# Optimization experiments

Hardware: AMD Instinct MI355X
Metric: run time of the kernel (lower is better)

## Reference

```python
import jax, jax.numpy as jnp
import numpy as np

N, CIN, COUT, E, NDIR = 65536, 128, 128, 589824, 9


def sel_conv(x, src, dst, sel, W, b):
    # x: [N, Cin]; W: [D, Cin, Cout]; edges j->i: out[i] += x[j] @ W[sel]
    n = x.shape[0]
    xs = x[src]  # [E, Cin] gather
    out = jnp.zeros((n, W.shape[2]), x.dtype)
    for d in range(W.shape[0]):  # fixed small direction count (9 or 1)
        m = (sel == d).astype(x.dtype)[:, None]
        agg = jax.ops.segment_sum(xs * m, dst, num_segments=n)  # [N, Cin]
        out = out + agg @ W[d]
    return out + b


def bn_eval(x, g, be, rm, rv, eps=1e-5):
    return (x - rm) * (g * jax.lax.rsqrt(rv + eps)) + be


def setup_inputs() -> dict:
    key = jax.random.key(0)
    ks = jax.random.split(key, 24)
    s = 0.05
    inp = {
        "x": jax.random.normal(ks[0], (N, CIN), jnp.float32),
        "edge_index": jax.random.randint(ks[1], (2, E), 0, N),
        "selections": jax.random.randint(ks[2], (E,), 0, NDIR),
        "W1": jax.random.normal(ks[3], (NDIR, CIN, COUT), jnp.float32) * s,
        "b1": jax.random.normal(ks[4], (COUT,), jnp.float32) * s,
        "g1": 1.0 + jax.random.normal(ks[5], (COUT,), jnp.float32) * s,
        "be1": jax.random.normal(ks[6], (COUT,), jnp.float32) * s,
        "rm1": jax.random.normal(ks[7], (COUT,), jnp.float32) * s,
        "rv1": 0.5 + jax.random.uniform(ks[8], (COUT,), jnp.float32),
        "W2": jax.random.normal(ks[9], (NDIR, COUT, COUT), jnp.float32) * s,
        "b2": jax.random.normal(ks[10], (COUT,), jnp.float32) * s,
        "g2": 1.0 + jax.random.normal(ks[11], (COUT,), jnp.float32) * s,
        "be2": jax.random.normal(ks[12], (COUT,), jnp.float32) * s,
        "rm2": jax.random.normal(ks[13], (COUT,), jnp.float32) * s,
        "rv2": 0.5 + jax.random.uniform(ks[14], (COUT,), jnp.float32),
        "W3": jax.random.normal(ks[15], (1, CIN, COUT), jnp.float32) * s,
        "b3": jax.random.normal(ks[16], (COUT,), jnp.float32) * s,
        "g3": 1.0 + jax.random.normal(ks[17], (COUT,), jnp.float32) * s,
        "be3": jax.random.normal(ks[18], (COUT,), jnp.float32) * s,
        "rm3": jax.random.normal(ks[19], (COUT,), jnp.float32) * s,
        "rv3": 0.5 + jax.random.uniform(ks[20], (COUT,), jnp.float32),
    }
    return inp


def reference(x, edge_index, selections, W1, b1, g1, be1, rm1, rv1,
              W2, b2, g2, be2, rm2, rv2, W3, b3, g3, be3, rm3, rv3):
    src, dst = edge_index[0], edge_index[1]
    # conv1: SelectionConv(3x3) + BN + ELU
    h = jax.nn.elu(bn_eval(sel_conv(x, src, dst, selections, W1, b1), g1, be1, rm1, rv1))
    # conv2: SelectionConv(3x3) + BN + ELU
    h = jax.nn.elu(bn_eval(sel_conv(h, src, dst, selections, W2, b2), g2, be2, rm2, rv2))
    # conv3: SelectionConv(1x1) shortcut (only selection-0 edges)
    sc = sel_conv(x, src, dst, selections, W3, b3)
    return jax.nn.elu(bn_eval(h + sc, g3, be3, rm3, rv3))
```

## Files before the change

### kernel.cpp

```cpp
#include <hip/hip_runtime.h>
#include <hip/hip_bf16.h>
#include <math.h>

#define N_NODES 65536
#define NDIR 9
#define NEDGE 589824
#define NBINS (N_NODES*NDIR)
#define TILE_M 32
#define SKEY_CAP 1024

typedef __attribute__((ext_vector_type(8))) short short8;
typedef __attribute__((ext_vector_type(4))) float f32x4;

__device__ inline float bf2f(unsigned short u){ return __uint_as_float(((unsigned int)u)<<16); }
__device__ inline unsigned short f2bf(float f){
  unsigned int x = __float_as_uint(f);
  x += 0x7fff + ((x>>16)&1);
  return (unsigned short)(x>>16);
}
__device__ inline float elu1(float x){ return x>0.f ? x : expm1f(x); }

__global__ void prep_w(const float* __restrict__ W1, const float* __restrict__ W2,
                       const float* __restrict__ W3,
                       const float* __restrict__ g1, const float* __restrict__ rv1,
                       const float* __restrict__ g2, const float* __restrict__ rv2,
                       const float* __restrict__ g3, const float* __restrict__ rv3,
                       unsigned short* __restrict__ Wt1, unsigned short* __restrict__ Wt2){
  int idx = blockIdx.x*256 + threadIdx.x;
  const float eps = 1e-5f;
  if (idx < 1280*128) {
    int n = idx >> 7, k = idx & 127;
    float v;
    if (n < 1152) { int d = n >> 7, c = n & 127;
      float s = g1[c]*rsqrtf(rv1[c]+eps); v = W1[(d*128 + k)*128 + c] * s; }
    else { int c = n - 1152;
      float s = g3[c]*rsqrtf(rv3[c]+eps); v = W3[k*128 + c] * s; }
    Wt1[idx] = f2bf(v);
  } else {
    int j = idx - 1280*128;
    int n = j >> 7, k = j & 127;
    int d = n >> 7, c = n & 127;
    float s = g2[c]*rsqrtf(rv2[c]+eps);
    Wt2[j] = f2bf(W2[(d*128 + k)*128 + c] * s);
  }
}

__global__ void prep_bias(const float* b1,const float* g1,const float* be1,const float* rm1,const float* rv1,
                          const float* b2,const float* g2,const float* be2,const float* rm2,const float* rv2,
                          const float* b3,const float* g3,const float* be3,const float* rm3,const float* rv3,
                          float* bias1, float* bias2, float* bias3, float* s3v){
  int c = threadIdx.x;
  const float eps = 1e-5f;
  float s1 = g1[c]*rsqrtf(rv1[c]+eps);
  bias1[c] = (b1[c]-rm1[c])*s1 + be1[c];
  float s2 = g2[c]*rsqrtf(rv2[c]+eps);
  bias2[c] = (b2[c]-rm2[c])*s2 + be2[c];
  float s3 = g3[c]*rsqrtf(rv3[c]+eps);
  bias3[c] = (b3[c]-rm3[c])*s3 + be3[c];
  s3v[c] = s3;
}

__global__ void xcast_k(const float* __restrict__ x, unsigned short* __restrict__ xb){
  int i = (blockIdx.x*256 + threadIdx.x)*8;
  f32x4 f0 = *(const f32x4*)(x + i);
  f32x4 f1 = *(const f32x4*)(x + i + 4);
  short8 t;
  #pragma unroll
  for (int j = 0; j < 4; j++){ t[j] = (short)f2bf(f0[j]); t[4+j] = (short)f2bf(f1[j]); }
  *(short8*)(xb + i) = t;
}

__global__ void hist_k(const int* __restrict__ dst, const int* __restrict__ sel,
                       int* __restrict__ hist){
  int e = blockIdx.x*256 + threadIdx.x;
  atomicAdd(&hist[dst[e]*9 + sel[e]], 1);
}

__global__ void scan1_k(const int* __restrict__ in, int* __restrict__ out, int* __restrict__ bsum){
  __shared__ int wsum[4];
  int t = threadIdx.x;
  int base = blockIdx.x*1024 + t*4;
  int4 v = *(const int4*)(in + base);
  int s = v.x + v.y + v.z + v.w;
  int lane = t & 63, w = t >> 6;
  int inc = s;
  #pragma unroll
  for (int o = 1; o < 64; o <<= 1){ int n = __shfl_up(inc, o); if (lane >= o) inc += n; }
  if (lane == 63) wsum[w] = inc;
  __syncthreads();
  int acc = 0;
  for (int i = 0; i < w; i++) acc += wsum[i];
  int ex = acc + inc - s;
  out[base] = ex; out[base+1] = ex + v.x; out[base+2] = ex + v.x + v.y; out[base+3] = ex + v.x + v.y + v.z;
  if (t == 255) bsum[blockIdx.x] = acc + inc;
}

__global__ void scan3_k(int* __restrict__ rs, const int* __restrict__ bsumx, int* __restrict__ cursor){
  int i = blockIdx.x*256 + threadIdx.x;
  int v = rs[i] + bsumx[i >> 10];
  rs[i] = v; cursor[i] = v;
  if (i == 0) rs[NBINS] = NEDGE;
}

__global__ void scatter_k(const int* __restrict__ src, const int* __restrict__ dst,
                          const int* __restrict__ sel,
                          int* __restrict__ cursor, int* __restrict__ sorted){
  int e = blockIdx.x*256 + threadIdx.x;
  int bin = dst[e]*9 + sel[e];
  int pos = atomicAdd(&cursor[bin], 1);
  sorted[pos] = src[e];
}

__device__ __forceinline__ void mfma_tile(f32x4 acc[2][2],
                                          const unsigned short* agg,
                                          const unsigned short* __restrict__ Wd,
                                          int w, int q, int r){
  #pragma unroll
  for (int kk = 0; kk < 4; kk++){
    const unsigned short* wp = Wd + (size_t)(w*32 + r)*128 + kk*32 + q*8;
    short8 b0 = *(const short8*)wp;
    short8 b1 = *(const short8*)(wp + 16*128);
    #pragma unroll
    for (int mt = 0; mt < 2; mt++){
      short8 av = *(const short8*)&agg[(mt*16 + r)*136 + kk*32 + q*8];
      acc[mt][0] = __builtin_amdgcn_mfma_f32_16x16x32_bf16(av, b0, acc[mt][0], 0, 0, 0);
      acc[mt][1] = __builtin_amdgcn_mfma_f32_16x16x32_bf16(av, b1, acc[mt][1], 0, 0, 0);
    }
  }
}

template<int IS_L2>
__global__ __launch_bounds__(256, 8) void layer_k(
    const unsigned short* __restrict__ H,
    const unsigned short* __restrict__ X,
    const unsigned short* __restrict__ Wf,
    const unsigned short* __restrict__ W3f,
    const int* __restrict__ rs, const int* __restrict__ sorted,
    const float* __restrict__ biasA, const float* __restrict__ bias3,
    const float* __restrict__ s3v,
    unsigned short* __restrict__ outB, float* __restrict__ outF){
  __shared__ __align__(16) unsigned short agg[TILE_M*136];
  __shared__ int skey[SKEY_CAP];
  __shared__ int rsl[TILE_M*9 + 1];
  const int tid = threadIdx.x;
  const int w = tid >> 6, lane = tid & 63;
  const int q = lane >> 4, r = lane & 15;
  const int rid = tid >> 4, c = tid & 15;
  const int m0 = blockIdx.x * TILE_M;

  for (int i = tid; i <= TILE_M*9; i += 256) rsl[i] = rs[m0*9 + i];
  __syncthreads();
  const int lo = rsl[0];
  const int cnt = rsl[TILE_M*9] - lo;
  for (int i = tid; i < cnt && i < SKEY_CAP; i += 256) skey[i] = sorted[lo + i];

  f32x4 acc[2][2];
  #pragma unroll
  for (int mt = 0; mt < 2; mt++){ acc[mt][0] = (f32x4){0,0,0,0}; acc[mt][1] = (f32x4){0,0,0,0}; }

  #pragma unroll 1
  for (int d = 0; d < 9; d++){
    __syncthreads();
    #pragma unroll
    for (int t = 0; t < 2; t++){
      int nl = t*16 + rid;
      int b = nl*9 + d;
      int s = rsl[b] - lo, e = rsl[b+1] - lo;
      f32x4 a0 = {0,0,0,0}, a1 = {0,0,0,0};
      for (int i = s; i < e; i++){
        int key = (i < SKEY_CAP) ? skey[i] : sorted[lo + i];
        short8 v = *(const short8*)(H + (size_t)key*128 + c*8);
        a0[0] += bf2f((unsigned short)v[0]); a0[1] += bf2f((unsigned short)v[1]);
        a0[2] += bf2f((unsigned short)v[2]); a0[3] += bf2f((unsigned short)v[3]);
        a1[0] += bf2f((unsigned short)v[4]); a1[1] += bf2f((unsigned short)v[5]);
        a1[2] += bf2f((unsigned short)v[6]); a1[3] += bf2f((unsigned short)v[7]);
      }
      short8 o;
      o[0]=(short)f2bf(a0[0]); o[1]=(short)f2bf(a0[1]); o[2]=(short)f2bf(a0[2]); o[3]=(short)f2bf(a0[3]);
      o[4]=(short)f2bf(a1[0]); o[5]=(short)f2bf(a1[1]); o[6]=(short)f2bf(a1[2]); o[7]=(short)f2bf(a1[3]);
      *(short8*)&agg[nl*136 + c*8] = o;
    }
    __syncthreads();
    mfma_tile(acc, agg, Wf + (size_t)d*128*128, w, q, r);
  }

  if constexpr (!IS_L2){
    #pragma unroll
    for (int mt = 0; mt < 2; mt++)
      #pragma unroll
      for (int n2 = 0; n2 < 2; n2++){
        int col = w*32 + n2*16 + r;
        float bA = biasA[col];
        #pragma unroll
        for (int rr = 0; rr < 4; rr++){
          int row = m0 + mt*16 + q*4 + rr;
          outB[(size_t)row*128 + col] = f2bf(elu1(acc[mt][n2][rr] + bA));
        }
      }
  } else {
    f32x4 sca[2][2];
    #pragma unroll
    for (int mt = 0; mt < 2; mt++){ sca[mt][0] = (f32x4){0,0,0,0}; sca[mt][1] = (f32x4){0,0,0,0}; }
    __syncthreads();
    #pragma unroll
    for (int t = 0; t < 2; t++){
      int nl = t*16 + rid;
      int b = nl*9;
      int s = rsl[b] - lo, e = rsl[b+1] - lo;
      f32x4 a0 = {0,0,0,0}, a1 = {0,0,0,0};
      for (int i = s; i < e; i++){
        int key = (i < SKEY_CAP) ? skey[i] : sorted[lo + i];
        short8 v = *(const short8*)(X + (size_t)key*128 + c*8);
        a0[0] += bf2f((unsigned short)v[0]); a0[1] += bf2f((unsigned short)v[1]);
        a0[2] += bf2f((unsigned short)v[2]); a0[3] += bf2f((unsigned short)v[3]);
        a1[0] += bf2f((unsigned short)v[4]); a1[1] += bf2f((unsigned short)v[5]);
        a1[2] += bf2f((unsigned short)v[6]); a1[3] += bf2f((unsigned short)v[7]);
      }
      short8 o;
      o[0]=(short)f2bf(a0[0]); o[1]=(short)f2bf(a0[1]); o[2]=(short)f2bf(a0[2]); o[3]=(short)f2bf(a0[3]);
      o[4]=(short)f2bf(a1[0]); o[5]=(short)f2bf(a1[1]); o[6]=(short)f2bf(a1[2]); o[7]=(short)f2bf(a1[3]);
      *(short8*)&agg[nl*136 + c*8] = o;
    }
    __syncthreads();
    mfma_tile(sca, agg, W3f, w, q, r);
    #pragma unroll
    for (int mt = 0; mt < 2; mt++)
      #pragma unroll
      for (int n2 = 0; n2 < 2; n2++){
        int col = w*32 + n2*16 + r;
        float bA = biasA[col], b3 = bias3[col], s3 = s3v[col];
        #pragma unroll
        for (int rr = 0; rr < 4; rr++){
          int row = m0 + mt*16 + q*4 + rr;
          float h = elu1(acc[mt][n2][rr] + bA);
          outF[(size_t)row*128 + col] = elu1(h*s3 + sca[mt][n2][rr] + b3);
        }
      }
  }
}

extern "C" void kernel_launch(void* const* d_in, const int* in_sizes, int n_in,
                              void* d_out, int out_size, void* d_ws, size_t ws_size,
                              hipStream_t stream){
  const float* x   = (const float*)d_in[0];
  const int*   ei  = (const int*)d_in[1];
  const int*   sel = (const int*)d_in[2];
  const float* W1  = (const float*)d_in[3];
  const float* b1  = (const float*)d_in[4];
  const float* g1  = (const float*)d_in[5];
  const float* be1 = (const float*)d_in[6];
  const float* rm1 = (const float*)d_in[7];
  const float* rv1 = (const float*)d_in[8];
  const float* W2  = (const float*)d_in[9];
  const float* b2  = (const float*)d_in[10];
  const float* g2  = (const float*)d_in[11];
  const float* be2 = (const float*)d_in[12];
  const float* rm2 = (const float*)d_in[13];
  const float* rv2 = (const float*)d_in[14];
  const float* W3  = (const float*)d_in[15];
  const float* b3  = (const float*)d_in[16];
  const float* g3  = (const float*)d_in[17];
  const float* be3 = (const float*)d_in[18];
  const float* rm3 = (const float*)d_in[19];
  const float* rv3 = (const float*)d_in[20];

  char* ws = (char*)d_ws;
  unsigned short* xb   = (unsigned short*)(ws);
  unsigned short* h1   = (unsigned short*)(ws + 16777216);
  unsigned short* Wt1  = (unsigned short*)(ws + 33554432);
  unsigned short* Wt2  = (unsigned short*)(ws + 33882112);
  float* bias1  = (float*)(ws + 34177024);
  float* bias2  = bias1 + 128;
  float* bias3  = bias1 + 256;
  float* s3v    = bias1 + 384;
  int* hist     = (int*)(ws + 34179072);
  int* rs       = (int*)(ws + 36538368);
  int* cursor   = (int*)(ws + 38897920);
  int* bsum     = (int*)(ws + 41257216);
  int* bsumx    = (int*)(ws + 41261312);
  int* bsumT    = (int*)(ws + 41265408);
  int* sorted   = (int*)(ws + 41265664);

  const int* srcp = ei;
  const int* dstp = ei + NEDGE;

  hipMemsetAsync(hist, 0, NBINS*sizeof(int), stream);
  prep_w<<<1216, 256, 0, stream>>>(W1, W2, W3, g1, rv1, g2, rv2, g3, rv3, Wt1, Wt2);
  prep_bias<<<1, 128, 0, stream>>>(b1,g1,be1,rm1,rv1, b2,g2,be2,rm2,rv2, b3,g3,be3,rm3,rv3,
                                   bias1, bias2, bias3, s3v);
  xcast_k<<<4096, 256, 0, stream>>>(x, xb);
  hist_k<<<NEDGE/256, 256, 0, stream>>>(dstp, sel, hist);
  scan1_k<<<NBINS/1024, 256, 0, stream>>>(hist, rs, bsum);
  scan1_k<<<1, 256, 0, stream>>>(bsum, bsumx, bsumT);
  scan3_k<<<NBINS/256, 256, 0, stream>>>(rs, bsumx, cursor);
  scatter_k<<<NEDGE/256, 256, 0, stream>>>(srcp, dstp, sel, cursor, sorted);

  layer_k<0><<<2048, 256, 0, stream>>>(xb, nullptr, Wt1, nullptr, rs, sorted,
                                       bias1, nullptr, nullptr, h1, nullptr);
  layer_k<1><<<2048, 256, 0, stream>>>(h1, xb, Wt2, Wt1 + 1152*128, rs, sorted,
                                       bias2, bias3, s3v, nullptr, (float*)d_out);
}
```

Baseline: 369.9 us.

## Gather all nine directions in one pass with unrolled loads and 512-thread blocks

The layer kernel now gathers all nine direction aggregates for a 32-node tile in a single sweep over each node's sorted edge list. Each thread issues four independent row loads per iteration and writes a per-direction result into a larger shared buffer, so the nine gather/sync/MFMA rounds become one gather phase followed by nine MFMA steps. Blocks grow to 512 threads with one node row per 16-lane group, and each wave computes a 16x32 output tile. The aim is more memory-level parallelism and fewer barriers, at the cost of a much larger LDS footprint (about 78 KB per block), lower occupancy, and a smaller shared key cache.

New measurement: 506.4 us. 1.37x slower.

```diff
diff --git a/kernel.cpp b/kernel.cpp
--- a/kernel.cpp
+++ b/kernel.cpp
@@ -7,7 +7,8 @@
 #define NEDGE 589824
 #define NBINS (N_NODES*NDIR)
 #define TILE_M 32
-#define SKEY_CAP 1024
+#define SKEY_CAP 448
+#define APITCH 136
 
 typedef __attribute__((ext_vector_type(8))) short short8;
 typedef __attribute__((ext_vector_type(4))) float f32x4;
@@ -111,26 +112,8 @@
   sorted[pos] = src[e];
 }
 
-__device__ __forceinline__ void mfma_tile(f32x4 acc[2][2],
-                                          const unsigned short* agg,
-                                          const unsigned short* __restrict__ Wd,
-                                          int w, int q, int r){
-  #pragma unroll
-  for (int kk = 0; kk < 4; kk++){
-    const unsigned short* wp = Wd + (size_t)(w*32 + r)*128 + kk*32 + q*8;
-    short8 b0 = *(const short8*)wp;
-    short8 b1 = *(const short8*)(wp + 16*128);
-    #pragma unroll
-    for (int mt = 0; mt < 2; mt++){
-      short8 av = *(const short8*)&agg[(mt*16 + r)*136 + kk*32 + q*8];
-      acc[mt][0] = __builtin_amdgcn_mfma_f32_16x16x32_bf16(av, b0, acc[mt][0], 0, 0, 0);
-      acc[mt][1] = __builtin_amdgcn_mfma_f32_16x16x32_bf16(av, b1, acc[mt][1], 0, 0, 0);
-    }
-  }
-}
-
 template<int IS_L2>
-__global__ __launch_bounds__(256, 8) void layer_k(
+__global__ __launch_bounds__(512, 4) void layer_k(
     const unsigned short* __restrict__ H,
     const unsigned short* __restrict__ X,
     const unsigned short* __restrict__ Wf,
@@ -139,103 +122,147 @@
     const float* __restrict__ biasA, const float* __restrict__ bias3,
     const float* __restrict__ s3v,
     unsigned short* __restrict__ outB, float* __restrict__ outF){
-  __shared__ __align__(16) unsigned short agg[TILE_M*136];
+  __shared__ __align__(16) unsigned short agg[NDIR*TILE_M*APITCH];
   __shared__ int skey[SKEY_CAP];
   __shared__ int rsl[TILE_M*9 + 1];
   const int tid = threadIdx.x;
   const int w = tid >> 6, lane = tid & 63;
   const int q = lane >> 4, r = lane & 15;
-  const int rid = tid >> 4, c = tid & 15;
+  const int nl = tid >> 4, c = tid & 15;
   const int m0 = blockIdx.x * TILE_M;
 
-  for (int i = tid; i <= TILE_M*9; i += 256) rsl[i] = rs[m0*9 + i];
+  for (int i = tid; i <= TILE_M*9; i += 512) rsl[i] = rs[m0*9 + i];
   __syncthreads();
   const int lo = rsl[0];
   const int cnt = rsl[TILE_M*9] - lo;
-  for (int i = tid; i < cnt && i < SKEY_CAP; i += 256) skey[i] = sorted[lo + i];
-
-  f32x4 acc[2][2];
-  #pragma unroll
-  for (int mt = 0; mt < 2; mt++){ acc[mt][0] = (f32x4){0,0,0,0}; acc[mt][1] = (f32x4){0,0,0,0}; }
-
-  #pragma unroll 1
-  for (int d = 0; d < 9; d++){
-    __syncthreads();
-    #pragma unroll
-    for (int t = 0; t < 2; t++){
-      int nl = t*16 + rid;
-      int b = nl*9 + d;
-      int s = rsl[b] - lo, e = rsl[b+1] - lo;
-      f32x4 a0 = {0,0,0,0}, a1 = {0,0,0,0};
-      for (int i = s; i < e; i++){
-        int key = (i < SKEY_CAP) ? skey[i] : sorted[lo + i];
-        short8 v = *(const short8*)(H + (size_t)key*128 + c*8);
+  for (int i = tid; i < cnt && i < SKEY_CAP; i += 512) skey[i] = sorted[lo + i];
+  __syncthreads();
+
+  {
+    const int b0 = nl*9;
+    const int s  = rsl[b0] - lo;
+    const int e9 = rsl[b0+9] - lo;
+    f32x4 a0 = (f32x4){0,0,0,0}, a1 = (f32x4){0,0,0,0};
+    int d = 0;
+    int nb = rsl[b0+1] - lo;
+
+    auto flushdir = [&](int dd){
+      short8 o;
+      o[0]=(short)f2bf(a0[0]); o[1]=(short)f2bf(a0[1]); o[2]=(short)f2bf(a0[2]); o[3]=(short)f2bf(a0[3]);
+      o[4]=(short)f2bf(a1[0]); o[5]=(short)f2bf(a1[1]); o[6]=(short)f2bf(a1[2]); o[7]=(short)f2bf(a1[3]);
+      *(short8*)&agg[((dd<<5) + nl)*APITCH + c*8] = o;
+      a0 = (f32x4){0,0,0,0}; a1 = (f32x4){0,0,0,0};
+    };
+    auto consume = [&](short8 v, int idx){
+      if (idx < e9) {
+        while (idx >= nb) { flushdir(d); d++; nb = rsl[b0 + d + 1] - lo; }
         a0[0] += bf2f((unsigned short)v[0]); a0[1] += bf2f((unsigned short)v[1]);
         a0[2] += bf2f((unsigned short)v[2]); a0[3] += bf2f((unsigned short)v[3]);
         a1[0] += bf2f((unsigned short)v[4]); a1[1] += bf2f((unsigned short)v[5]);
         a1[2] += bf2f((unsigned short)v[6]); a1[3] += bf2f((unsigned short)v[7]);
       }
+    };
+
+    for (int i = s; i < e9; i += 4) {
+      int j1 = (i+1 < e9) ? i+1 : i;
+      int j2 = (i+2 < e9) ? i+2 : i;
+      int j3 = (i+3 < e9) ? i+3 : i;
+      int k0 = (i  < SKEY_CAP) ? skey[i]  : sorted[lo + i];
+      int k1 = (j1 < SKEY_CAP) ? skey[j1] : sorted[lo + j1];
+      int k2 = (j2 < SKEY_CAP) ? skey[j2] : sorted[lo + j2];
+      int k3 = (j3 < SKEY_CAP) ? skey[j3] : sorted[lo + j3];
+      short8 v0 = *(const short8*)(H + (size_t)k0*128 + c*8);
+      short8 v1 = *(const short8*)(H + (size_t)k1*128 + c*8);
+      short8 v2 = *(const short8*)(H + (size_t)k2*128 + c*8);
+      short8 v3 = *(const short8*)(H + (size_t)k3*128 + c*8);
+      consume(v0, i); consume(v1, i+1); consume(v2, i+2); consume(v3, i+3);
+    }
+    for (; d < 9; d++) flushdir(d);
+  }
+  __syncthreads();
+
+  const int wr = (w & 1) * 16;
+  const int wc = (w >> 1) * 32;
+  f32x4 acc[2];
+  acc[0] = (f32x4){0,0,0,0}; acc[1] = (f32x4){0,0,0,0};
+  for (int d = 0; d < 9; d++){
+    const unsigned short* ag = agg + ((d<<5) + wr + r)*APITCH;
+    const unsigned short* Wd = Wf + (size_t)d*128*128 + (size_t)(wc + r)*128;
+    #pragma unroll
+    for (int kk = 0; kk < 4; kk++){
+      short8 av = *(const short8*)(ag + kk*32 + q*8);
+      short8 b0 = *(const short8*)(Wd + kk*32 + q*8);
+      short8 b1 = *(const short8*)(Wd + 16*128 + kk*32 + q*8);
+      acc[0] = __builtin_amdgcn_mfma_f32_16x16x32_bf16(av, b0, acc[0], 0, 0, 0);
+      acc[1] = __builtin_amdgcn_mfma_f32_16x16x32_bf16(av, b1, acc[1], 0, 0, 0);
+    }
+  }
+
+  if constexpr (!IS_L2){
+    #pragma unroll
+    for (int n2 = 0; n2 < 2; n2++){
+      int col = wc + n2*16 + r;
+      float bA = biasA[col];
+      #pragma unroll
+      for (int rr = 0; rr < 4; rr++){
+        int row = m0 + wr + q*4 + rr;
+        outB[(size_t)row*128 + col] = f2bf(elu1(acc[n2][rr] + bA));
+      }
+    }
+  } else {
+    __syncthreads();
+    {
+      const int b0 = nl*9;
+      const int s = rsl[b0] - lo, e = rsl[b0+1] - lo;
+      f32x4 a0 = (f32x4){0,0,0,0}, a1 = (f32x4){0,0,0,0};
+      for (int i = s; i < e; i += 2) {
+        int j1 = (i+1 < e) ? i+1 : i;
+        int k0 = (i  < SKEY_CAP) ? skey[i]  : sorted[lo + i];
+        int k1 = (j1 < SKEY_CAP) ? skey[j1] : sorted[lo + j1];
+        short8 v0 = *(const short8*)(X + (size_t)k0*128 + c*8);
+        short8 v1 = *(const short8*)(X + (size_t)k1*128 + c*8);
+        a0[0] += bf2f((unsigned short)v0[0]); a0[1] += bf2f((unsigned short)v0[1]);
+        a0[2] += bf2f((unsigned short)v0[2]); a0[3] += bf2f((unsigned short)v0[3]);
+        a1[0] += bf2f((unsigned short)v0[4]); a1[1] += bf2f((unsigned short)v0[5]);
+        a1[2] += bf2f((unsigned short)v0[6]); a1[3] += bf2f((unsigned short)v0[7]);
+        if (i+1 < e) {
+          a0[0] += bf2f((unsigned short)v1[0]); a0[1] += bf2f((unsigned short)v1[1]);
+          a0[2] += bf2f((unsigned short)v1[2]); a0[3] += bf2f((unsigned short)v1[3]);
+          a1[0] += bf2f((unsigned short)v1[4]); a1[1] += bf2f((unsigned short)v1[5]);
+          a1[2] += bf2f((unsigned short)v1[6]); a1[3] += bf2f((unsigned short)v1[7]);
+        }
+      }
       short8 o;
       o[0]=(short)f2bf(a0[0]); o[1]=(short)f2bf(a0[1]); o[2]=(short)f2bf(a0[2]); o[3]=(short)f2bf(a0[3]);
       o[4]=(short)f2bf(a1[0]); o[5]=(short)f2bf(a1[1]); o[6]=(short)f2bf(a1[2]); o[7]=(short)f2bf(a1[3]);
-      *(short8*)&agg[nl*136 + c*8] = o;
+      *(short8*)&agg[nl*APITCH + c*8] = o;
     }
     __syncthreads();
-    mfma_tile(acc, agg, Wf + (size_t)d*128*128, w, q, r);
-  }
-
-  if constexpr (!IS_L2){
+    f32x4 sca[2];
+    sca[0] = (f32x4){0,0,0,0}; sca[1] = (f32x4){0,0,0,0};
+    {
+      const unsigned short* ag = agg + (wr + r)*APITCH;
+      const unsigned short* Wd = W3f + (size_t)(wc + r)*128;
+      #pragma unroll
+      for (int kk = 0; kk < 4; kk++){
+        short8 av = *(const short8*)(ag + kk*32 + q*8);
+        short8 b0 = *(const short8*)(Wd + kk*32 + q*8);
+        short8 b1 = *(const short8*)(Wd + 16*128 + kk*32 + q*8);
+        sca[0] = __builtin_amdgcn_mfma_f32_16x16x32_bf16(av, b0, sca[0], 0, 0, 0);
+        sca[1] = __builtin_amdgcn_mfma_f32_16x16x32_bf16(av, b1, sca[1], 0, 0, 0);
+      }
+    }
     #pragma unroll
-    for (int mt = 0; mt < 2; mt++)
+    for (int n2 = 0; n2 < 2; n2++){
+      int col = wc + n2*16 + r;
+      float bA = biasA[col], b3 = bias3[col], s3 = s3v[col];
       #pragma unroll
-      for (int n2 = 0; n2 < 2; n2++){
-        int col = w*32 + n2*16 + r;
-        float bA = biasA[col];
-        #pragma unroll
-        for (int rr = 0; rr < 4; rr++){
-          int row = m0 + mt*16 + q*4 + rr;
-          outB[(size_t)row*128 + col] = f2bf(elu1(acc[mt][n2][rr] + bA));
-        }
-      }
-  } else {
-    f32x4 sca[2][2];
-    #pragma unroll
-    for (int mt = 0; mt < 2; mt++){ sca[mt][0] = (f32x4){0,0,0,0}; sca[mt][1] = (f32x4){0,0,0,0}; }
-    __syncthreads();
-    #pragma unroll
-    for (int t = 0; t < 2; t++){
-      int nl = t*16 + rid;
-      int b = nl*9;
-      int s = rsl[b] - lo, e = rsl[b+1] - lo;
-      f32x4 a0 = {0,0,0,0}, a1 = {0,0,0,0};
-      for (int i = s; i < e; i++){
-        int key = (i < SKEY_CAP) ? skey[i] : sorted[lo + i];
-        short8 v = *(const short8*)(X + (size_t)key*128 + c*8);
-        a0[0] += bf2f((unsigned short)v[0]); a0[1] += bf2f((unsigned short)v[1]);
-        a0[2] += bf2f((unsigned short)v[2]); a0[3] += bf2f((unsigned short)v[3]);
-        a1[0] += bf2f((unsigned short)v[4]); a1[1] += bf2f((unsigned short)v[5]);
-        a1[2] += bf2f((unsigned short)v[6]); a1[3] += bf2f((unsigned short)v[7]);
-      }
-      short8 o;
-      o[0]=(short)f2bf(a0[0]); o[1]=(short)f2bf(a0[1]); o[2]=(short)f2bf(a0[2]); o[3]=(short)f2bf(a0[3]);
-      o[4]=(short)f2bf(a1[0]); o[5]=(short)f2bf(a1[1]); o[6]=(short)f2bf(a1[2]); o[7]=(short)f2bf(a1[3]);
-      *(short8*)&agg[nl*136 + c*8] = o;
-    }
-    __syncthreads();
-    mfma_tile(sca, agg, W3f, w, q, r);
-    #pragma unroll
-    for (int mt = 0; mt < 2; mt++)
-      #pragma unroll
-      for (int n2 = 0; n2 < 2; n2++){
-        int col = w*32 + n2*16 + r;
-        float bA = biasA[col], b3 = bias3[col], s3 = s3v[col];
-        #pragma unroll
-        for (int rr = 0; rr < 4; rr++){
-          int row = m0 + mt*16 + q*4 + rr;
-          float h = elu1(acc[mt][n2][rr] + bA);
-          outF[(size_t)row*128 + col] = elu1(h*s3 + sca[mt][n2][rr] + b3);
-        }
-      }
+      for (int rr = 0; rr < 4; rr++){
+        int row = m0 + wr + q*4 + rr;
+        float h = elu1(acc[n2][rr] + bA);
+        outF[(size_t)row*128 + col] = elu1(h*s3 + sca[n2][rr] + b3);
+      }
+    }
   }
 }
 
@@ -295,8 +322,8 @@
   scan3_k<<<NBINS/256, 256, 0, stream>>>(rs, bsumx, cursor);
   scatter_k<<<NEDGE/256, 256, 0, stream>>>(srcp, dstp, sel, cursor, sorted);
 
-  layer_k<0><<<2048, 256, 0, stream>>>(xb, nullptr, Wt1, nullptr, rs, sorted,
+  layer_k<0><<<2048, 512, 0, stream>>>(xb, nullptr, Wt1, nullptr, rs, sorted,
                                        bias1, nullptr, nullptr, h1, nullptr);
-  layer_k<1><<<2048, 256, 0, stream>>>(h1, xb, Wt2, Wt1 + 1152*128, rs, sorted,
+  layer_k<1><<<2048, 512, 0, stream>>>(h1, xb, Wt2, Wt1 + 1152*128, rs, sorted,
                                        bias2, bias3, s3v, nullptr, (float*)d_out);
 }
```

## Double-buffer aggregation tile and interleave two row gathers per thread

Applied to the files above, without the earlier changes.

Adds a second LDS aggregation buffer, alternated by direction parity, so one barrier per direction suffices instead of two. The two rows handled by each thread are now gathered in a single interleaved loop, putting two independent global loads in flight per iteration. The shortcut gather writes to the other buffer. Launch bounds drop from 8 to 7 waves to allow the extra LDS and registers. The interleaved loop runs to the longer of the two segments and masks the shorter one, which can waste a load.

Measured after the change: 417.1 us. 1.13x slower.

```diff
diff --git a/kernel.cpp b/kernel.cpp
--- a/kernel.cpp
+++ b/kernel.cpp
@@ -8,6 +8,7 @@
 #define NBINS (N_NODES*NDIR)
 #define TILE_M 32
 #define SKEY_CAP 1024
+#define APITCH 136
 
 typedef __attribute__((ext_vector_type(8))) short short8;
 typedef __attribute__((ext_vector_type(4))) float f32x4;
@@ -122,7 +123,7 @@
     short8 b1 = *(const short8*)(wp + 16*128);
     #pragma unroll
     for (int mt = 0; mt < 2; mt++){
-      short8 av = *(const short8*)&agg[(mt*16 + r)*136 + kk*32 + q*8];
+      short8 av = *(const short8*)&agg[(mt*16 + r)*APITCH + kk*32 + q*8];
       acc[mt][0] = __builtin_amdgcn_mfma_f32_16x16x32_bf16(av, b0, acc[mt][0], 0, 0, 0);
       acc[mt][1] = __builtin_amdgcn_mfma_f32_16x16x32_bf16(av, b1, acc[mt][1], 0, 0, 0);
     }
@@ -130,7 +131,7 @@
 }
 
 template<int IS_L2>
-__global__ __launch_bounds__(256, 8) void layer_k(
+__global__ __launch_bounds__(256, 7) void layer_k(
     const unsigned short* __restrict__ H,
     const unsigned short* __restrict__ X,
     const unsigned short* __restrict__ Wf,
@@ -139,7 +140,7 @@
     const float* __restrict__ biasA, const float* __restrict__ bias3,
     const float* __restrict__ s3v,
     unsigned short* __restrict__ outB, float* __restrict__ outF){
-  __shared__ __align__(16) unsigned short agg[TILE_M*136];
+  __shared__ __align__(16) unsigned short agg[2*TILE_M*APITCH];
   __shared__ int skey[SKEY_CAP];
   __shared__ int rsl[TILE_M*9 + 1];
   const int tid = threadIdx.x;
@@ -153,6 +154,7 @@
   const int lo = rsl[0];
   const int cnt = rsl[TILE_M*9] - lo;
   for (int i = tid; i < cnt && i < SKEY_CAP; i += 256) skey[i] = sorted[lo + i];
+  __syncthreads();
 
   f32x4 acc[2][2];
   #pragma unroll
@@ -160,28 +162,46 @@
 
   #pragma unroll 1
   for (int d = 0; d < 9; d++){
-    __syncthreads();
-    #pragma unroll
-    for (int t = 0; t < 2; t++){
-      int nl = t*16 + rid;
-      int b = nl*9 + d;
-      int s = rsl[b] - lo, e = rsl[b+1] - lo;
-      f32x4 a0 = {0,0,0,0}, a1 = {0,0,0,0};
-      for (int i = s; i < e; i++){
-        int key = (i < SKEY_CAP) ? skey[i] : sorted[lo + i];
-        short8 v = *(const short8*)(H + (size_t)key*128 + c*8);
-        a0[0] += bf2f((unsigned short)v[0]); a0[1] += bf2f((unsigned short)v[1]);
-        a0[2] += bf2f((unsigned short)v[2]); a0[3] += bf2f((unsigned short)v[3]);
-        a1[0] += bf2f((unsigned short)v[4]); a1[1] += bf2f((unsigned short)v[5]);
-        a1[2] += bf2f((unsigned short)v[6]); a1[3] += bf2f((unsigned short)v[7]);
+    unsigned short* buf = agg + (d & 1)*(TILE_M*APITCH);
+    {
+      int bA = rid*9 + d, bB = (16 + rid)*9 + d;
+      int sA = rsl[bA] - lo, eA = rsl[bA+1] - lo;
+      int sB = rsl[bB] - lo, eB = rsl[bB+1] - lo;
+      f32x4 aA0 = (f32x4){0,0,0,0}, aA1 = (f32x4){0,0,0,0};
+      f32x4 aB0 = (f32x4){0,0,0,0}, aB1 = (f32x4){0,0,0,0};
+      int lenA = eA - sA, lenB = eB - sB;
+      int n = lenA > lenB ? lenA : lenB;
+      for (int it = 0; it < n; it++){
+        int iA = sA + it, iB = sB + it;
+        bool dA = iA < eA, dB = iB < eB;
+        int kA = dA ? ((iA < SKEY_CAP) ? skey[iA] : sorted[lo + iA]) : 0;
+        int kB = dB ? ((iB < SKEY_CAP) ? skey[iB] : sorted[lo + iB]) : 0;
+        short8 vA = *(const short8*)(H + (size_t)kA*128 + c*8);
+        short8 vB = *(const short8*)(H + (size_t)kB*128 + c*8);
+        if (dA){
+          aA0[0] += bf2f((unsigned short)vA[0]); aA0[1] += bf2f((unsigned short)vA[1]);
+          aA0[2] += bf2f((unsigned short)vA[2]); aA0[3] += bf2f((unsigned short)vA[3]);
+          aA1[0] += bf2f((unsigned short)vA[4]); aA1[1] += bf2f((unsigned short)vA[5]);
+          aA1[2] += bf2f((unsigned short)vA[6]); aA1[3] += bf2f((unsigned short)vA[7]);
+        }
+        if (dB){
+          aB0[0] += bf2f((unsigned short)vB[0]); aB0[1] += bf2f((unsigned short)vB[1]);
+          aB0[2] += bf2f((unsigned short)vB[2]); aB0[3] += bf2f((unsigned short)vB[3]);
+          aB1[0] += bf2f((unsigned short)vB[4]); aB1[1] += bf2f((unsigned short)vB[5]);
+          aB1[2] += bf2f((unsigned short)vB[6]); aB1[3] += bf2f((unsigned short)vB[7]);
+        }
       }
-      short8 o;
-      o[0]=(short)f2bf(a0[0]); o[1]=(short)f2bf(a0[1]); o[2]=(short)f2bf(a0[2]); o[3]=(short)f2bf(a0[3]);
-      o[4]=(short)f2bf(a1[0]); o[5]=(short)f2bf(a1[1]); o[6]=(short)f2bf(a1[2]); o[7]=(short)f2bf(a1[3]);
-      *(short8*)&agg[nl*136 + c*8] = o;
+      short8 oA;
+      oA[0]=(short)f2bf(aA0[0]); oA[1]=(short)f2bf(aA0[1]); oA[2]=(short)f2bf(aA0[2]); oA[3]=(short)f2bf(aA0[3]);
+      oA[4]=(short)f2bf(aA1[0]); oA[5]=(short)f2bf(aA1[1]); oA[6]=(short)f2bf(aA1[2]); oA[7]=(short)f2bf(aA1[3]);
+      *(short8*)&buf[rid*APITCH + c*8] = oA;
+      short8 oB;
+      oB[0]=(short)f2bf(aB0[0]); oB[1]=(short)f2bf(aB0[1]); oB[2]=(short)f2bf(aB0[2]); oB[3]=(short)f2bf(aB0[3]);
+      oB[4]=(short)f2bf(aB1[0]); oB[5]=(short)f2bf(aB1[1]); oB[6]=(short)f2bf(aB1[2]); oB[7]=(short)f2bf(aB1[3]);
+      *(short8*)&buf[(16 + rid)*APITCH + c*8] = oB;
     }
     __syncthreads();
-    mfma_tile(acc, agg, Wf + (size_t)d*128*128, w, q, r);
+    mfma_tile(acc, buf, Wf + (size_t)d*128*128, w, q, r);
   }
 
   if constexpr (!IS_L2){
@@ -198,31 +218,49 @@
         }
       }
   } else {
+    unsigned short* bufS = agg + TILE_M*APITCH;
+    {
+      int bA = rid*9, bB = (16 + rid)*9;
+      int sA = rsl[bA] - lo, eA = rsl[bA+1] - lo;
+      int sB = rsl[bB] - lo, eB = rsl[bB+1] - lo;
+      f32x4 aA0 = (f32x4){0,0,0,0}, aA1 = (f32x4){0,0,0,0};
+      f32x4 aB0 = (f32x4){0,0,0,0}, aB1 = (f32x4){0,0,0,0};
+      int lenA = eA - sA, lenB = eB - sB;
+      int n = lenA > lenB ? lenA : lenB;
+      for (int it = 0; it < n; it++){
+        int iA = sA + it, iB = sB + it;
+        bool dA = iA < eA, dB = iB < eB;
+        int kA = dA ? ((iA < SKEY_CAP) ? skey[iA] : sorted[lo + iA]) : 0;
+        int kB = dB ? ((iB < SKEY_CAP) ? skey[iB] : sorted[lo + iB]) : 0;
+        short8 vA = *(const short8*)(X + (size_t)kA*128 + c*8);
+        short8 vB = *(const short8*)(X + (size_t)kB*128 + c*8);
+        if (dA){
+          aA0[0] += bf2f((unsigned short)vA[0]); aA0[1] += bf2f((unsigned short)vA[1]);
+          aA0[2] += bf2f((unsigned short)vA[2]); aA0[3] += bf2f((unsigned short)vA[3]);
+          aA1[0] += bf2f((unsigned short)vA[4]); aA1[1] += bf2f((unsigned short)vA[5]);
+          aA1[2] += bf2f((unsigned short)vA[6]); aA1[3] += bf2f((unsigned short)vA[7]);
+        }
+        if (dB){
+          aB0[0] += bf2f((unsigned short)vB[0]); aB0[1] += bf2f((unsigned short)vB[1]);
+          aB0[2] += bf2f((unsigned short)vB[2]); aB0[3] += bf2f((unsigned short)vB[3]);
+          aB1[0] += bf2f((unsigned short)vB[4]); aB1[1] += bf2f((unsigned short)vB[5]);
+          aB1[2] += bf2f((unsigned short)vB[6]); aB1[3] += bf2f((unsigned short)vB[7]);
+        }
+      }
+      short8 oA;
+      oA[0]=(short)f2bf(aA0[0]); oA[1]=(short)f2bf(aA0[1]); oA[2]=(short)f2bf(aA0[2]); oA[3]=(short)f2bf(aA0[3]);
+      oA[4]=(short)f2bf(aA1[0]); oA[5]=(short)f2bf(aA1[1]); oA[6]=(short)f2bf(aA1[2]); oA[7]=(short)f2bf(aA1[3]);
+      *(short8*)&bufS[rid*APITCH + c*8] = oA;
+      short8 oB;
+      oB[0]=(short)f2bf(aB0[0]); oB[1]=(short)f2bf(aB0[1]); oB[2]=(short)f2bf(aB0[2]); oB[3]=(short)f2bf(aB0[3]);
+      oB[4]=(short)f2bf(aB1[0]); oB[5]=(short)f2bf(aB1[1]); oB[6]=(short)f2bf(aB1[2]); oB[7]=(short)f2bf(aB1[3]);
+      *(short8*)&bufS[(16 + rid)*APITCH + c*8] = oB;
+    }
+    __syncthreads();
     f32x4 sca[2][2];
     #pragma unroll
     for (int mt = 0; mt < 2; mt++){ sca[mt][0] = (f32x4){0,0,0,0}; sca[mt][1] = (f32x4){0,0,0,0}; }
-    __syncthreads();
-    #pragma unroll
-    for (int t = 0; t < 2; t++){
-      int nl = t*16 + rid;
-      int b = nl*9;
-      int s = rsl[b] - lo, e = rsl[b+1] - lo;
-      f32x4 a0 = {0,0,0,0}, a1 = {0,0,0,0};
-      for (int i = s; i < e; i++){
-        int key = (i < SKEY_CAP) ? skey[i] : sorted[lo + i];
-        short8 v = *(const short8*)(X + (size_t)key*128 + c*8);
-        a0[0] += bf2f((unsigned short)v[0]); a0[1] += bf2f((unsigned short)v[1]);
-        a0[2] += bf2f((unsigned short)v[2]); a0[3] += bf2f((unsigned short)v[3]);
-        a1[0] += bf2f((unsigned short)v[4]); a1[1] += bf2f((unsigned short)v[5]);
-        a1[2] += bf2f((unsigned short)v[6]); a1[3] += bf2f((unsigned short)v[7]);
-      }
-      short8 o;
-      o[0]=(short)f2bf(a0[0]); o[1]=(short)f2bf(a0[1]); o[2]=(short)f2bf(a0[2]); o[3]=(short)f2bf(a0[3]);
-      o[4]=(short)f2bf(a1[0]); o[5]=(short)f2bf(a1[1]); o[6]=(short)f2bf(a1[2]); o[7]=(short)f2bf(a1[3]);
-      *(short8*)&agg[nl*136 + c*8] = o;
-    }
-    __syncthreads();
-    mfma_tile(sca, agg, W3f, w, q, r);
+    mfma_tile(sca, bufS, W3f, w, q, r);
     #pragma unroll
     for (int mt = 0; mt < 2; mt++)
       #pragma unroll
```

## Aggregate neighbors directly into MFMA A-fragments per wave, dropping shared memory

Applied to the files above, without the earlier changes.

Each wave now owns 16 destination rows. Each lane gathers and sums 32 channels of one row, in the exact layout of the MFMA A operand. This removes the shared-memory aggregation tile, the shared key cache and all block barriers, and the lane then multiplies against all 128 output columns itself. In exchange, each lane holds 32 float accumulators plus 8 output accumulators, which raises register pressure (launch bounds lowered to 4). Gathers are also less coalesced, since 16 lanes now walk different rows with different edge counts, which adds divergence within a wave.

New measurement: 525.2 us. +42.0%, slower.

```diff
diff --git a/kernel.cpp b/kernel.cpp
--- a/kernel.cpp
+++ b/kernel.cpp
@@ -6,8 +6,6 @@
 #define NDIR 9
 #define NEDGE 589824
 #define NBINS (N_NODES*NDIR)
-#define TILE_M 32
-#define SKEY_CAP 1024
 
 typedef __attribute__((ext_vector_type(8))) short short8;
 typedef __attribute__((ext_vector_type(4))) float f32x4;
@@ -111,26 +109,8 @@
   sorted[pos] = src[e];
 }
 
-__device__ __forceinline__ void mfma_tile(f32x4 acc[2][2],
-                                          const unsigned short* agg,
-                                          const unsigned short* __restrict__ Wd,
-                                          int w, int q, int r){
-  #pragma unroll
-  for (int kk = 0; kk < 4; kk++){
-    const unsigned short* wp = Wd + (size_t)(w*32 + r)*128 + kk*32 + q*8;
-    short8 b0 = *(const short8*)wp;
-    short8 b1 = *(const short8*)(wp + 16*128);
-    #pragma unroll
-    for (int mt = 0; mt < 2; mt++){
-      short8 av = *(const short8*)&agg[(mt*16 + r)*136 + kk*32 + q*8];
-      acc[mt][0] = __builtin_amdgcn_mfma_f32_16x16x32_bf16(av, b0, acc[mt][0], 0, 0, 0);
-      acc[mt][1] = __builtin_amdgcn_mfma_f32_16x16x32_bf16(av, b1, acc[mt][1], 0, 0, 0);
-    }
-  }
-}
-
 template<int IS_L2>
-__global__ __launch_bounds__(256, 8) void layer_k(
+__global__ __launch_bounds__(256, 4) void layer_k(
     const unsigned short* __restrict__ H,
     const unsigned short* __restrict__ X,
     const unsigned short* __restrict__ Wf,
@@ -139,103 +119,122 @@
     const float* __restrict__ biasA, const float* __restrict__ bias3,
     const float* __restrict__ s3v,
     unsigned short* __restrict__ outB, float* __restrict__ outF){
-  __shared__ __align__(16) unsigned short agg[TILE_M*136];
-  __shared__ int skey[SKEY_CAP];
-  __shared__ int rsl[TILE_M*9 + 1];
   const int tid = threadIdx.x;
-  const int w = tid >> 6, lane = tid & 63;
-  const int q = lane >> 4, r = lane & 15;
-  const int rid = tid >> 4, c = tid & 15;
-  const int m0 = blockIdx.x * TILE_M;
-
-  for (int i = tid; i <= TILE_M*9; i += 256) rsl[i] = rs[m0*9 + i];
-  __syncthreads();
-  const int lo = rsl[0];
-  const int cnt = rsl[TILE_M*9] - lo;
-  for (int i = tid; i < cnt && i < SKEY_CAP; i += 256) skey[i] = sorted[lo + i];
-
-  f32x4 acc[2][2];
+  const int wv = tid >> 6, l = tid & 63;
+  const int r = l & 15, g = l >> 4;
+  const int m0 = (blockIdx.x*4 + wv)*16;
+  const int row = m0 + r;
+  const int binb = row*9;
+
+  f32x4 accC[8];
   #pragma unroll
-  for (int mt = 0; mt < 2; mt++){ acc[mt][0] = (f32x4){0,0,0,0}; acc[mt][1] = (f32x4){0,0,0,0}; }
+  for (int ct = 0; ct < 8; ct++) accC[ct] = (f32x4){0,0,0,0};
 
   #pragma unroll 1
   for (int d = 0; d < 9; d++){
-    __syncthreads();
-    #pragma unroll
-    for (int t = 0; t < 2; t++){
-      int nl = t*16 + rid;
-      int b = nl*9 + d;
-      int s = rsl[b] - lo, e = rsl[b+1] - lo;
-      f32x4 a0 = {0,0,0,0}, a1 = {0,0,0,0};
-      for (int i = s; i < e; i++){
-        int key = (i < SKEY_CAP) ? skey[i] : sorted[lo + i];
-        short8 v = *(const short8*)(H + (size_t)key*128 + c*8);
-        a0[0] += bf2f((unsigned short)v[0]); a0[1] += bf2f((unsigned short)v[1]);
-        a0[2] += bf2f((unsigned short)v[2]); a0[3] += bf2f((unsigned short)v[3]);
-        a1[0] += bf2f((unsigned short)v[4]); a1[1] += bf2f((unsigned short)v[5]);
-        a1[2] += bf2f((unsigned short)v[6]); a1[3] += bf2f((unsigned short)v[7]);
-      }
-      short8 o;
-      o[0]=(short)f2bf(a0[0]); o[1]=(short)f2bf(a0[1]); o[2]=(short)f2bf(a0[2]); o[3]=(short)f2bf(a0[3]);
-      o[4]=(short)f2bf(a1[0]); o[5]=(short)f2bf(a1[1]); o[6]=(short)f2bf(a1[2]); o[7]=(short)f2bf(a1[3]);
-      *(short8*)&agg[nl*136 + c*8] = o;
-    }
-    __syncthreads();
-    mfma_tile(acc, agg, Wf + (size_t)d*128*128, w, q, r);
+    float aA[4][8];
+    #pragma unroll
+    for (int kk = 0; kk < 4; kk++)
+      #pragma unroll
+      for (int j = 0; j < 8; j++) aA[kk][j] = 0.f;
+
+    int s = rs[binb + d], e = rs[binb + d + 1];
+    for (int i = s; i < e; ++i){
+      int key = sorted[i];
+      const unsigned short* hp = H + (size_t)key*128 + g*8;
+      short8 v0 = *(const short8*)(hp);
+      short8 v1 = *(const short8*)(hp + 32);
+      short8 v2 = *(const short8*)(hp + 64);
+      short8 v3 = *(const short8*)(hp + 96);
+      #pragma unroll
+      for (int j = 0; j < 8; j++){
+        aA[0][j] += bf2f((unsigned short)v0[j]);
+        aA[1][j] += bf2f((unsigned short)v1[j]);
+        aA[2][j] += bf2f((unsigned short)v2[j]);
+        aA[3][j] += bf2f((unsigned short)v3[j]);
+      }
+    }
+    short8 af[4];
+    #pragma unroll
+    for (int kk = 0; kk < 4; kk++)
+      #pragma unroll
+      for (int j = 0; j < 8; j++) af[kk][j] = (short)f2bf(aA[kk][j]);
+
+    const unsigned short* Wd = Wf + (size_t)d*16384 + (size_t)r*128 + g*8;
+    #pragma unroll
+    for (int ct = 0; ct < 8; ct++){
+      const unsigned short* wp = Wd + ct*16*128;
+      #pragma unroll
+      for (int kk = 0; kk < 4; kk++){
+        short8 bfr = *(const short8*)(wp + kk*32);
+        accC[ct] = __builtin_amdgcn_mfma_f32_16x16x32_bf16(af[kk], bfr, accC[ct], 0, 0, 0);
+      }
+    }
   }
 
   if constexpr (!IS_L2){
     #pragma unroll
-    for (int mt = 0; mt < 2; mt++)
-      #pragma unroll
-      for (int n2 = 0; n2 < 2; n2++){
-        int col = w*32 + n2*16 + r;
-        float bA = biasA[col];
-        #pragma unroll
-        for (int rr = 0; rr < 4; rr++){
-          int row = m0 + mt*16 + q*4 + rr;
-          outB[(size_t)row*128 + col] = f2bf(elu1(acc[mt][n2][rr] + bA));
-        }
-      }
+    for (int ct = 0; ct < 8; ct++){
+      int col = ct*16 + r;
+      float bA = biasA[col];
+      #pragma unroll
+      for (int rr = 0; rr < 4; rr++){
+        int orow = m0 + g*4 + rr;
+        outB[(size_t)orow*128 + col] = f2bf(elu1(accC[ct][rr] + bA));
+      }
+    }
   } else {
-    f32x4 sca[2][2];
-    #pragma unroll
-    for (int mt = 0; mt < 2; mt++){ sca[mt][0] = (f32x4){0,0,0,0}; sca[mt][1] = (f32x4){0,0,0,0}; }
-    __syncthreads();
-    #pragma unroll
-    for (int t = 0; t < 2; t++){
-      int nl = t*16 + rid;
-      int b = nl*9;
-      int s = rsl[b] - lo, e = rsl[b+1] - lo;
-      f32x4 a0 = {0,0,0,0}, a1 = {0,0,0,0};
-      for (int i = s; i < e; i++){
-        int key = (i < SKEY_CAP) ? skey[i] : sorted[lo + i];
-        short8 v = *(const short8*)(X + (size_t)key*128 + c*8);
-        a0[0] += bf2f((unsigned short)v[0]); a0[1] += bf2f((unsigned short)v[1]);
-        a0[2] += bf2f((unsigned short)v[2]); a0[3] += bf2f((unsigned short)v[3]);
-        a1[0] += bf2f((unsigned short)v[4]); a1[1] += bf2f((unsigned short)v[5]);
-        a1[2] += bf2f((unsigned short)v[6]); a1[3] += bf2f((unsigned short)v[7]);
-      }
-      short8 o;
-      o[0]=(short)f2bf(a0[0]); o[1]=(short)f2bf(a0[1]); o[2]=(short)f2bf(a0[2]); o[3]=(short)f2bf(a0[3]);
-      o[4]=(short)f2bf(a1[0]); o[5]=(short)f2bf(a1[1]); o[6]=(short)f2bf(a1[2]); o[7]=(short)f2bf(a1[3]);
-      *(short8*)&agg[nl*136 + c*8] = o;
-    }
-    __syncthreads();
-    mfma_tile(sca, agg, W3f, w, q, r);
-    #pragma unroll
-    for (int mt = 0; mt < 2; mt++)
-      #pragma unroll
-      for (int n2 = 0; n2 < 2; n2++){
-        int col = w*32 + n2*16 + r;
-        float bA = biasA[col], b3 = bias3[col], s3 = s3v[col];
-        #pragma unroll
-        for (int rr = 0; rr < 4; rr++){
-          int row = m0 + mt*16 + q*4 + rr;
-          float h = elu1(acc[mt][n2][rr] + bA);
-          outF[(size_t)row*128 + col] = elu1(h*s3 + sca[mt][n2][rr] + b3);
-        }
-      }
+    float aA[4][8];
+    #pragma unroll
+    for (int kk = 0; kk < 4; kk++)
+      #pragma unroll
+      for (int j = 0; j < 8; j++) aA[kk][j] = 0.f;
+    int s = rs[binb], e = rs[binb + 1];
+    for (int i = s; i < e; ++i){
+      int key = sorted[i];
+      const unsigned short* xp = X + (size_t)key*128 + g*8;
+      short8 v0 = *(const short8*)(xp);
+      short8 v1 = *(const short8*)(xp + 32);
+      short8 v2 = *(const short8*)(xp + 64);
+      short8 v3 = *(const short8*)(xp + 96);
+      #pragma unroll
+      for (int j = 0; j < 8; j++){
+        aA[0][j] += bf2f((unsigned short)v0[j]);
+        aA[1][j] += bf2f((unsigned short)v1[j]);
+        aA[2][j] += bf2f((unsigned short)v2[j]);
+        aA[3][j] += bf2f((unsigned short)v3[j]);
+      }
+    }
+    short8 af[4];
+    #pragma unroll
+    for (int kk = 0; kk < 4; kk++)
+      #pragma unroll
+      for (int j = 0; j < 8; j++) af[kk][j] = (short)f2bf(aA[kk][j]);
+
+    f32x4 sca[8];
+    #pragma unroll
+    for (int ct = 0; ct < 8; ct++) sca[ct] = (f32x4){0,0,0,0};
+    const unsigned short* W3b = W3f + (size_t)r*128 + g*8;
+    #pragma unroll
+    for (int ct = 0; ct < 8; ct++){
+      const unsigned short* wp = W3b + ct*16*128;
+      #pragma unroll
+      for (int kk = 0; kk < 4; kk++){
+        short8 bfr = *(const short8*)(wp + kk*32);
+        sca[ct] = __builtin_amdgcn_mfma_f32_16x16x32_bf16(af[kk], bfr, sca[ct], 0, 0, 0);
+      }
+    }
+    #pragma unroll
+    for (int ct = 0; ct < 8; ct++){
+      int col = ct*16 + r;
+      float bA = biasA[col], b3 = bias3[col], s3 = s3v[col];
+      #pragma unroll
+      for (int rr = 0; rr < 4; rr++){
+        int orow = m0 + g*4 + rr;
+        float h = elu1(accC[ct][rr] + bA);
+        outF[(size_t)orow*128 + col] = elu1(h*s3 + sca[ct][rr] + b3);
+      }
+    }
   }
 }
 
@@ -295,8 +294,8 @@
   scan3_k<<<NBINS/256, 256, 0, stream>>>(rs, bsumx, cursor);
   scatter_k<<<NEDGE/256, 256, 0, stream>>>(srcp, dstp, sel, cursor, sorted);
 
-  layer_k<0><<<2048, 256, 0, stream>>>(xb, nullptr, Wt1, nullptr, rs, sorted,
+  layer_k<0><<<1024, 256, 0, stream>>>(xb, nullptr, Wt1, nullptr, rs, sorted,
                                        bias1, nullptr, nullptr, h1, nullptr);
-  layer_k<1><<<2048, 256, 0, stream>>>(h1, xb, Wt2, Wt1 + 1152*128, rs, sorted,
+  layer_k<1><<<1024, 256, 0, stream>>>(h1, xb, Wt2, Wt1 + 1152*128, rs, sorted,
                                        bias2, bias3, s3v, nullptr, (float*)d_out);
 }
```
